# Performance work log

Hardware: AMD Instinct MI355X
Metric: run time of the kernel (lower is better)

## Reference

```python
import jax, jax.numpy as jnp
import numpy as np
from jax import lax

B, C_IN, C_OUT, K, W, H = 2, 64, 64, 9, 192, 192
EXTEND_SCOPE = 1.0
EPS = 1e-5
GN_GROUPS = C_OUT // 4


def setup_inputs() -> dict:
    key = jax.random.key(0)
    ks = jax.random.split(key, 6)
    f = jax.random.normal(ks[0], (B, C_IN, W, H), jnp.float32)
    offset_w = jax.random.normal(ks[1], (2 * K, C_IN, 3, 3), jnp.float32) * 0.02
    offset_b = jax.random.normal(ks[2], (2 * K,), jnp.float32) * 0.02
    bn_gamma = jnp.ones((2 * K,), jnp.float32)
    bn_beta = jnp.zeros((2 * K,), jnp.float32)
    conv_w = jax.random.normal(ks[3], (C_OUT, C_IN, K, 1), jnp.float32) * 0.05
    conv_b = jax.random.normal(ks[4], (C_OUT,), jnp.float32) * 0.05
    gn_gamma = jnp.ones((C_OUT,), jnp.float32)
    gn_beta = jnp.zeros((C_OUT,), jnp.float32)
    return dict(f=f, offset_w=offset_w, offset_b=offset_b, bn_gamma=bn_gamma,
                bn_beta=bn_beta, conv_w=conv_w, conv_b=conv_b,
                gn_gamma=gn_gamma, gn_beta=gn_beta)


def _forward(f, offset_w, offset_b, bn_gamma, bn_beta, conv_w, conv_b, gn_gamma, gn_beta):
    # --- offset branch: 3x3 conv -> eval-mode BatchNorm -> tanh ---
    off = lax.conv_general_dilated(f, offset_w, (1, 1), [(1, 1), (1, 1)],
                                   dimension_numbers=('NCHW', 'OIHW', 'NCHW'))
    off = off + offset_b[None, :, None, None]
    # BN eval: running_mean=0, running_var=1
    off = off / jnp.sqrt(1.0 + EPS) * bn_gamma[None, :, None, None] + bn_beta[None, :, None, None]
    off = jnp.tanh(off)
    y_off = off[:, :K]  # [B,K,W,H]; x_off (off[:, K:]) is unused when morph == 0

    # --- cumulative snake offsets along the kernel axis (morph=0 uses y only) ---
    center = K // 2
    # faithful to source: tensor starts as a detached clone; entries never
    # reassigned by the loop (index 0 and K-1 for odd K) keep raw detached offsets
    new = [lax.stop_gradient(y_off[:, i]) for i in range(K)]
    new[center] = jnp.zeros_like(new[center])
    for j in range(1, center):
        new[center + j] = new[center + j - 1] + y_off[:, center + j]
        new[center - j] = new[center - j + 1] + y_off[:, center - j]
    y_off_cum = jnp.stack(new, axis=1)  # [B,K,W,H]

    # --- deformed sampling coordinates ---
    w_idx = jnp.arange(W, dtype=jnp.float32)[None, None, :, None]
    h_idx = jnp.arange(H, dtype=jnp.float32)[None, None, None, :]
    k_off = (jnp.arange(K, dtype=jnp.float32) - center)[None, :, None, None]
    y_new = w_idx + EXTEND_SCOPE * y_off_cum              # [B,K,W,H]
    x_new = jnp.broadcast_to(h_idx + k_off, (B, K, W, H))  # [B,K,W,H]
    # torch layout: [B,K,W,H] -> [B,W,K,H] -> [B, K*W, H]
    yf = y_new.transpose(0, 2, 1, 3).reshape(-1)
    xf = x_new.transpose(0, 2, 1, 3).reshape(-1)

    # --- bilinear interpolation gather ---
    y0 = jnp.floor(yf)
    x0 = jnp.floor(xf)
    y0i = jnp.clip(y0.astype(jnp.int32), 0, W - 1)
    y1i = jnp.clip(y0.astype(jnp.int32) + 1, 0, W - 1)
    x0i = jnp.clip(x0.astype(jnp.int32), 0, H - 1)
    x1i = jnp.clip(x0.astype(jnp.int32) + 1, 0, H - 1)

    # faithful to source: base batch offset cancels, so every batch gathers
    # from batch 0's feature map
    feat0 = f[0].transpose(1, 2, 0).reshape(W * H, C_IN)  # [(w,h), C]
    va0 = feat0[y0i * H + x0i]
    vc0 = feat0[y0i * H + x1i]
    va1 = feat0[y1i * H + x0i]
    vc1 = feat0[y1i * H + x1i]

    # interpolation weights use the looser clamp [0, W] / [0, H] (source behavior)
    y0w = jnp.clip(y0, 0.0, float(W))
    y1w = jnp.clip(y0 + 1.0, 0.0, float(W))
    x0w = jnp.clip(x0, 0.0, float(H))
    x1w = jnp.clip(x0 + 1.0, 0.0, float(H))
    wa0 = (y1w - yf) * (x1w - xf)
    wc0 = (y1w - yf) * (xf - x0w)
    wa1 = (yf - y0w) * (x1w - xf)
    wc1 = (yf - y0w) * (xf - x0w)
    vals = va0 * wa0[:, None] + vc0 * wc0[:, None] + va1 * wa1[:, None] + vc1 * wc1[:, None]
    deformed = vals.reshape(B, K * W, H, C_IN).transpose(0, 3, 1, 2)  # [B,C,K*W,H]

    # --- dsc_conv_x: (K,1) kernel, (K,1) stride -> [B,C_out,W,H] ---
    z = lax.conv_general_dilated(deformed, conv_w, (K, 1), 'VALID',
                                 dimension_numbers=('NCHW', 'OIHW', 'NCHW'))
    z = z + conv_b[None, :, None, None]

    # --- GroupNorm(out_ch//4, out_ch) + ReLU ---
    zg = z.reshape(B, GN_GROUPS, -1)
    mu = zg.mean(axis=-1, keepdims=True)
    var = zg.var(axis=-1, keepdims=True)
    zg = (zg - mu) / jnp.sqrt(var + EPS)
    z = zg.reshape(B, C_OUT, W, H) * gn_gamma[None, :, None, None] + gn_beta[None, :, None, None]
    return jax.nn.relu(z)


def reference(f, offset_w, offset_b, bn_gamma, bn_beta, conv_w, conv_b, gn_gamma, gn_beta):
    return _forward(f, offset_w, offset_b, bn_gamma, bn_beta, conv_w, conv_b, gn_gamma, gn_beta)
```

## Files before the change

kernel.cpp:

```cpp
#include <hip/hip_runtime.h>

#define BB 2
#define CIN 64
#define COUT 64
#define KK 9
#define WW 192
#define HH 192
#define WH (WW*HH)
#define CENTER 4
#define NT 32
#define DEFP 584
#define GROUPS 16
constexpr float EPSV = 1e-5f;
constexpr int NPERG = 4 * WH;

typedef __attribute__((ext_vector_type(8))) short short8v;
typedef __attribute__((ext_vector_type(4))) float float4v;

__device__ __forceinline__ float bf2f(unsigned short u) {
    union { unsigned int i; float f; } x; x.i = ((unsigned int)u) << 16; return x.f;
}
__device__ __forceinline__ unsigned short f2bf(float f) {
    union { float f; unsigned int i; } x; x.f = f;
    unsigned int i = x.i;
    unsigned int r = i + 0x7FFFu + ((i >> 16) & 1u);
    return (unsigned short)(r >> 16);
}

__global__ void k_prep(const float* __restrict__ cw, const float* __restrict__ ow,
                       unsigned short* __restrict__ wtA, float* __restrict__ wl_g)
{
    int i = blockIdx.x * 256 + threadIdx.x;
    if (i < COUT * CIN * KK) {
        int o = i / 576, ck = i % 576;
        int k = ck >> 6, c = ck & 63;
        wtA[i] = f2bf(cw[o * 576 + c * 9 + k]);
    }
    int j2 = i - COUT * CIN * KK;
    if (j2 >= 0 && j2 < CIN * 9 * 12) {
        int c = j2 / 108, rem = j2 % 108, tap = rem / 12, jj = rem % 12;
        wl_g[j2] = (jj < 9) ? ow[jj * 576 + c * 9 + tap] : 0.f;
    }
}

__global__ __launch_bounds__(256) void k_tr(const float* __restrict__ f,
                                            unsigned short* __restrict__ f_t)
{
    __shared__ unsigned short tile[64][72];
    int tid = threadIdx.x;
    int y = blockIdx.y;
    int x0 = blockIdx.x * 64;
    int xl = tid & 63, cq = tid >> 6;
#pragma unroll
    for (int ci = 0; ci < 16; ++ci) {
        int c = cq * 16 + ci;
        tile[xl][c] = f2bf(f[c * WH + y * HH + x0 + xl]);
    }
    __syncthreads();
    int cp = tid & 31, xr0 = tid >> 5;
#pragma unroll
    for (int xi = 0; xi < 8; ++xi) {
        int xr = xr0 * 8 + xi;
        unsigned int val = (unsigned int)tile[xr][2 * cp] |
                           ((unsigned int)tile[xr][2 * cp + 1] << 16);
        ((unsigned int*)f_t)[(y * HH + x0 + xr) * 32 + cp] = val;
    }
}

__global__ __launch_bounds__(512) void k_offset(
    const float* __restrict__ f, const float* __restrict__ wl_g,
    const float* __restrict__ ob, const float* __restrict__ bg,
    const float* __restrict__ bb, float* __restrict__ ycum)
{
    __shared__ float4 wl4[1728];
    __shared__ float sacc[64 * 73];
    float* wl = (float*)wl4;

    int tid = threadIdx.x;
    for (int i = tid; i < 1728; i += 512)
        wl4[i] = ((const float4*)wl_g)[i];

    int hl = tid & 63, ch = tid >> 6;
    int h = blockIdx.x * 64 + hl;
    int w = blockIdx.y, b = blockIdx.z;
    __syncthreads();

    float acc[9];
#pragma unroll
    for (int j = 0; j < 9; ++j) acc[j] = 0.f;

    const float* fb = f + ((size_t)b * CIN + ch * 8) * WH;
    for (int ci = 0; ci < 8; ++ci) {
        const float* fc = fb + ci * WH;
        const float* wp = wl + (ch * 8 + ci) * 108;
#pragma unroll
        for (int dw = 0; dw < 3; ++dw) {
            int r = w + dw - 1;
            if ((unsigned)r >= WW) continue;
            const float* fr_ = fc + r * HH;
#pragma unroll
            for (int dh = 0; dh < 3; ++dh) {
                int cl = h + dh - 1;
                if ((unsigned)cl >= HH) continue;
                float v = fr_[cl];
                const float* ww = wp + (dw * 3 + dh) * 12;
                float4 wa = *(const float4*)ww;
                float4 wb2 = *(const float4*)(ww + 4);
                float w8 = ww[8];
                acc[0] += v * wa.x;  acc[1] += v * wa.y;
                acc[2] += v * wa.z;  acc[3] += v * wa.w;
                acc[4] += v * wb2.x; acc[5] += v * wb2.y;
                acc[6] += v * wb2.z; acc[7] += v * wb2.w;
                acc[8] += v * w8;
            }
        }
    }
#pragma unroll
    for (int j = 0; j < 9; ++j)
        sacc[hl * 73 + ch * 9 + j] = acc[j];
    __syncthreads();

    if (tid < 64) {
        float s[9];
#pragma unroll
        for (int j = 0; j < 9; ++j) {
            float t0 = 0.f;
#pragma unroll
            for (int c = 0; c < 8; ++c) t0 += sacc[tid * 73 + c * 9 + j];
            s[j] = t0;
        }
        const float inv = 1.0f / sqrtf(1.0f + EPSV);
        float t[9];
#pragma unroll
        for (int j = 0; j < 9; ++j)
            t[j] = tanhf((s[j] + ob[j]) * inv * bg[j] + bb[j]);
        float cum[9];
        cum[4] = 0.f;
        cum[5] = t[5]; cum[6] = cum[5] + t[6]; cum[7] = cum[6] + t[7];
        cum[3] = t[3]; cum[2] = cum[3] + t[2]; cum[1] = cum[2] + t[1];
        cum[0] = t[0]; cum[8] = t[8];
        int hh = blockIdx.x * 64 + tid;
#pragma unroll
        for (int j = 0; j < 9; ++j)
            ycum[((b * KK + j) * WW + w) * HH + hh] = cum[j];
    }
}

__global__ __launch_bounds__(256) void k_main(
    const unsigned short* __restrict__ f_t, const float* __restrict__ ycum,
    const unsigned short* __restrict__ wtA, const float* __restrict__ cb,
    float* __restrict__ zout)
{
    __shared__ unsigned short def[NT * DEFP];
    __shared__ short m_y0[KK * NT], m_y1[KK * NT], m_x[KK * NT];
    __shared__ float m_w0[KK * NT], m_w1[KK * NT];

    int tid = threadIdx.x;
    int h0blk = blockIdx.x * NT;
    int w = blockIdx.y;
    int b = blockIdx.z;
    int lane = tid & 63;
    int wid = tid >> 6;
    int lr = lane & 15;
    int lg = lane >> 4;
    int o0 = wid * 16;

    short8v afr[18];
    const unsigned short* wbase = wtA + (o0 + lr) * 576 + lg * 8;
#pragma unroll
    for (int s = 0; s < 18; ++s)
        afr[s] = *(const short8v*)(wbase + s * 32);

    for (int p = tid; p < KK * NT; p += 256) {
        int k = p / NT;
        int hl = p % NT;
        int h = h0blk + hl;
        float yf = ycum[((b * KK + k) * WW + w) * HH + h] + (float)w;
        int x = h + k - CENTER;
        float y0f = floorf(yf);
        int iy0 = (int)y0f;
        int y0i = min(max(iy0, 0), WW - 1);
        int y1i = min(max(iy0 + 1, 0), WW - 1);
        float y0w = fminf(fmaxf(y0f, 0.f), (float)WW);
        float y1w = fminf(fmaxf(y0f + 1.f, 0.f), (float)WW);
        float w0 = y1w - yf;
        float w1 = yf - y0w;
        if (x < 0 || x >= HH) { w0 = 0.f; w1 = 0.f; }
        m_y0[p] = (short)y0i;
        m_y1[p] = (short)y1i;
        m_x[p]  = (short)min(max(x, 0), HH - 1);
        m_w0[p] = w0;
        m_w1[p] = w1;
    }
    __syncthreads();

    for (int it = tid; it < KK * NT * 4; it += 256) {
        int q = it & 3;
        int p = it >> 2;
        int y0i = m_y0[p], y1i = m_y1[p], x = m_x[p];
        float w0 = m_w0[p], w1 = m_w1[p];
        const unsigned short* r0 = f_t + ((y0i * HH + x) << 6) + q * 16;
        const unsigned short* r1 = f_t + ((y1i * HH + x) << 6) + q * 16;
        short8v a0 = *(const short8v*)r0;
        short8v a1 = *(const short8v*)(r0 + 8);
        short8v c0 = *(const short8v*)r1;
        short8v c1 = *(const short8v*)(r1 + 8);
        short8v o0v, o1v;
#pragma unroll
        for (int c = 0; c < 8; ++c) {
            float v0 = bf2f((unsigned short)a0[c]) * w0 + bf2f((unsigned short)c0[c]) * w1;
            float v1 = bf2f((unsigned short)a1[c]) * w0 + bf2f((unsigned short)c1[c]) * w1;
            o0v[c] = (short)f2bf(v0);
            o1v[c] = (short)f2bf(v1);
        }
        int hl = p & 31;
        int k = p >> 5;
        unsigned short* d = &def[hl * DEFP + k * 64 + q * 16];
        *(short8v*)d = o0v;
        *(short8v*)(d + 8) = o1v;
    }
    __syncthreads();

    float4v acc0 = {0.f, 0.f, 0.f, 0.f};
    float4v acc1 = {0.f, 0.f, 0.f, 0.f};
    const unsigned short* drow0 = &def[lr * DEFP + lg * 8];
    const unsigned short* drow1 = &def[(16 + lr) * DEFP + lg * 8];
#pragma unroll
    for (int s = 0; s < 18; ++s) {
        short8v b0 = *(const short8v*)(drow0 + s * 32);
        short8v b1 = *(const short8v*)(drow1 + s * 32);
        acc0 = __builtin_amdgcn_mfma_f32_16x16x32_bf16(afr[s], b0, acc0, 0, 0, 0);
        acc1 = __builtin_amdgcn_mfma_f32_16x16x32_bf16(afr[s], b1, acc1, 0, 0, 0);
    }

    float4 cbv = *(const float4*)(cb + o0 + lg * 4);
    size_t base = ((size_t)(b * COUT + o0 + lg * 4) * WW + w) * HH + h0blk + lr;
#pragma unroll
    for (int r = 0; r < 4; ++r) {
        float bias = (r == 0) ? cbv.x : (r == 1) ? cbv.y : (r == 2) ? cbv.z : cbv.w;
        zout[base + (size_t)r * WH]      = acc0[r] + bias;
        zout[base + (size_t)r * WH + 16] = acc1[r] + bias;
    }
}

__global__ __launch_bounds__(1024) void k_gstats(const float* __restrict__ z,
                                                 float* __restrict__ ms)
{
    __shared__ float sL[16], qL[16];
    int b = blockIdx.x >> 4, g = blockIdx.x & 15;
    const float4* p = (const float4*)(z + ((size_t)b * COUT + g * 4) * WH);
    float s = 0.f, q = 0.f;
    for (int i = threadIdx.x; i < WH; i += 1024) {
        float4 v = p[i];
        s += v.x + v.y + v.z + v.w;
        q += v.x * v.x + v.y * v.y + v.z * v.z + v.w * v.w;
    }
#pragma unroll
    for (int m = 1; m < 64; m <<= 1) {
        s += __shfl_xor(s, m);
        q += __shfl_xor(q, m);
    }
    int wv = threadIdx.x >> 6;
    if ((threadIdx.x & 63) == 0) { sL[wv] = s; qL[wv] = q; }
    __syncthreads();
    if (threadIdx.x == 0) {
        float ts = 0.f, tq = 0.f;
#pragma unroll
        for (int i = 0; i < 16; ++i) { ts += sL[i]; tq += qL[i]; }
        float mean = ts / (float)NPERG;
        float var = tq / (float)NPERG - mean * mean;
        ms[b * GROUPS + g] = mean;
        ms[BB * GROUPS + b * GROUPS + g] = 1.0f / sqrtf(var + EPSV);
    }
}

__global__ __launch_bounds__(256) void k_norm(
    float* __restrict__ z, const float* __restrict__ ms,
    const float* __restrict__ gg, const float* __restrict__ gb)
{
    int i = blockIdx.x * 256 + threadIdx.x;
    const int total4 = BB * COUT * WH / 4;
    if (i >= total4) return;
    float4 v = ((float4*)z)[i];
    int idx = i * 4;
    int o = (idx / WH) % COUT;
    int b = idx / (COUT * WH);
    int g = o >> 2;
    float mean = ms[b * GROUPS + g];
    float istd = ms[BB * GROUPS + b * GROUPS + g];
    float ga = gg[o], be = gb[o];
    v.x = fmaxf((v.x - mean) * istd * ga + be, 0.f);
    v.y = fmaxf((v.y - mean) * istd * ga + be, 0.f);
    v.z = fmaxf((v.z - mean) * istd * ga + be, 0.f);
    v.w = fmaxf((v.w - mean) * istd * ga + be, 0.f);
    ((float4*)z)[i] = v;
}

extern "C" void kernel_launch(void* const* d_in, const int* in_sizes, int n_in,
                              void* d_out, int out_size, void* d_ws, size_t ws_size,
                              hipStream_t stream)
{
    const float* f  = (const float*)d_in[0];
    const float* ow = (const float*)d_in[1];
    const float* ob = (const float*)d_in[2];
    const float* bg = (const float*)d_in[3];
    const float* bb = (const float*)d_in[4];
    const float* cw = (const float*)d_in[5];
    const float* cb = (const float*)d_in[6];
    const float* gg = (const float*)d_in[7];
    const float* gb = (const float*)d_in[8];
    float* out = (float*)d_out;

    char* ws = (char*)d_ws;
    unsigned short* f_t  = (unsigned short*)ws;
    float* ycum          = (float*)(ws + 4718592);
    unsigned short* wtA  = (unsigned short*)(ws + 4718592 + 2654208);
    float* wl_g          = (float*)(ws + 4718592 + 2654208 + 73728);
    float* ms            = (float*)(ws + 4718592 + 2654208 + 73728 + 27648);

    k_prep<<<(36864 + 6912 + 255) / 256, 256, 0, stream>>>(cw, ow, wtA, wl_g);
    k_tr<<<dim3(3, WW), 256, 0, stream>>>(f, f_t);
    k_offset<<<dim3(3, WW, BB), 512, 0, stream>>>(f, wl_g, ob, bg, bb, ycum);
    k_main<<<dim3(HH / NT, WW, BB), 256, 0, stream>>>(f_t, ycum, wtA, cb, out);
    k_gstats<<<BB * GROUPS, 1024, 0, stream>>>(out, ms);
    k_norm<<<(BB * COUT * WH / 4 + 255) / 256, 256, 0, stream>>>(out, ms, gg, gb);
}
```

Measured before the change: 198.7 us.

## Fuse offset conv into deformable sampling kernel, dropping ycum buffer

Merges the offset-branch 3x3 conv with BN, tanh and cumulative sum into the main sampling+MFMA kernel. Each 32-column tile now computes its own offsets and feeds the sampling coordinates straight into shared memory, so the ycum global round trip and one kernel launch go away. The offset partial sums reuse the def shared buffer as scratch. The cost is more work per block and higher shared memory and register pressure, which may lower occupancy. Offset conv parallelism also changes from 64 to 32 columns per block with 8 channel groups.

```diff
diff --git a/kernel.cpp b/kernel.cpp
--- a/kernel.cpp
+++ b/kernel.cpp
@@ -67,66 +67,78 @@
     }
 }
 
-__global__ __launch_bounds__(512) void k_offset(
-    const float* __restrict__ f, const float* __restrict__ wl_g,
+__global__ __launch_bounds__(256) void k_fused(
+    const float* __restrict__ f, const unsigned short* __restrict__ f_t,
+    const float* __restrict__ wl_g, const unsigned short* __restrict__ wtA,
     const float* __restrict__ ob, const float* __restrict__ bg,
-    const float* __restrict__ bb, float* __restrict__ ycum)
+    const float* __restrict__ bb, const float* __restrict__ cb,
+    float* __restrict__ zout)
 {
     __shared__ float4 wl4[1728];
-    __shared__ float sacc[64 * 73];
+    __shared__ unsigned short def[NT * DEFP];
+    __shared__ short m_y0[KK * NT], m_y1[KK * NT], m_x[KK * NT];
+    __shared__ float m_w0[KK * NT], m_w1[KK * NT];
     float* wl = (float*)wl4;
+    float* part = (float*)def;
 
     int tid = threadIdx.x;
-    for (int i = tid; i < 1728; i += 512)
+    int h0 = blockIdx.x * NT;
+    int w = blockIdx.y;
+    int b = blockIdx.z;
+    int lane = tid & 63;
+    int wid = tid >> 6;
+    int lr = lane & 15;
+    int lg = lane >> 4;
+    int o0 = wid * 16;
+
+    for (int i = tid; i < 1728; i += 256)
         wl4[i] = ((const float4*)wl_g)[i];
 
-    int hl = tid & 63, ch = tid >> 6;
-    int h = blockIdx.x * 64 + hl;
-    int w = blockIdx.y, b = blockIdx.z;
-    __syncthreads();
-
+    int p = tid & 31, c8 = tid >> 5;
     float acc[9];
 #pragma unroll
     for (int j = 0; j < 9; ++j) acc[j] = 0.f;
-
-    const float* fb = f + ((size_t)b * CIN + ch * 8) * WH;
-    for (int ci = 0; ci < 8; ++ci) {
-        const float* fc = fb + ci * WH;
-        const float* wp = wl + (ch * 8 + ci) * 108;
-#pragma unroll
-        for (int dw = 0; dw < 3; ++dw) {
-            int r = w + dw - 1;
-            if ((unsigned)r >= WW) continue;
-            const float* fr_ = fc + r * HH;
-#pragma unroll
-            for (int dh = 0; dh < 3; ++dh) {
-                int cl = h + dh - 1;
-                if ((unsigned)cl >= HH) continue;
-                float v = fr_[cl];
-                const float* ww = wp + (dw * 3 + dh) * 12;
-                float4 wa = *(const float4*)ww;
-                float4 wb2 = *(const float4*)(ww + 4);
-                float w8 = ww[8];
-                acc[0] += v * wa.x;  acc[1] += v * wa.y;
-                acc[2] += v * wa.z;  acc[3] += v * wa.w;
-                acc[4] += v * wb2.x; acc[5] += v * wb2.y;
-                acc[6] += v * wb2.z; acc[7] += v * wb2.w;
-                acc[8] += v * w8;
-            }
+    const float* fb = f + ((size_t)b * CIN + c8 * 8) * WH;
+    __syncthreads();
+
+#pragma unroll
+    for (int tap = 0; tap < 9; ++tap) {
+        int r = w + tap / 3 - 1;
+        int cl = h0 + p + tap % 3 - 1;
+        if ((unsigned)r >= WW || (unsigned)cl >= HH) continue;
+        const float* src = fb + r * HH + cl;
+#pragma unroll
+        for (int cc = 0; cc < 8; ++cc) {
+            float v = src[cc * WH];
+            const float* ww = wl + (c8 * 8 + cc) * 108 + tap * 12;
+            float4 wa = *(const float4*)ww;
+            float4 wb2 = *(const float4*)(ww + 4);
+            float w8 = ww[8];
+            acc[0] += v * wa.x;  acc[1] += v * wa.y;
+            acc[2] += v * wa.z;  acc[3] += v * wa.w;
+            acc[4] += v * wb2.x; acc[5] += v * wb2.y;
+            acc[6] += v * wb2.z; acc[7] += v * wb2.w;
+            acc[8] += v * w8;
         }
     }
 #pragma unroll
     for (int j = 0; j < 9; ++j)
-        sacc[hl * 73 + ch * 9 + j] = acc[j];
-    __syncthreads();
-
-    if (tid < 64) {
+        part[(c8 * 32 + p) * 9 + j] = acc[j];
+
+    short8v afr[18];
+    const unsigned short* wbase = wtA + (o0 + lr) * 576 + lg * 8;
+#pragma unroll
+    for (int s = 0; s < 18; ++s)
+        afr[s] = *(const short8v*)(wbase + s * 32);
+    __syncthreads();
+
+    if (tid < NT) {
         float s[9];
 #pragma unroll
         for (int j = 0; j < 9; ++j) {
             float t0 = 0.f;
 #pragma unroll
-            for (int c = 0; c < 8; ++c) t0 += sacc[tid * 73 + c * 9 + j];
+            for (int g = 0; g < 8; ++g) t0 += part[(g * 32 + tid) * 9 + j];
             s[j] = t0;
         }
         const float inv = 1.0f / sqrtf(1.0f + EPSV);
@@ -139,66 +151,35 @@
         cum[5] = t[5]; cum[6] = cum[5] + t[6]; cum[7] = cum[6] + t[7];
         cum[3] = t[3]; cum[2] = cum[3] + t[2]; cum[1] = cum[2] + t[1];
         cum[0] = t[0]; cum[8] = t[8];
-        int hh = blockIdx.x * 64 + tid;
-#pragma unroll
-        for (int j = 0; j < 9; ++j)
-            ycum[((b * KK + j) * WW + w) * HH + hh] = cum[j];
-    }
-}
-
-__global__ __launch_bounds__(256) void k_main(
-    const unsigned short* __restrict__ f_t, const float* __restrict__ ycum,
-    const unsigned short* __restrict__ wtA, const float* __restrict__ cb,
-    float* __restrict__ zout)
-{
-    __shared__ unsigned short def[NT * DEFP];
-    __shared__ short m_y0[KK * NT], m_y1[KK * NT], m_x[KK * NT];
-    __shared__ float m_w0[KK * NT], m_w1[KK * NT];
-
-    int tid = threadIdx.x;
-    int h0blk = blockIdx.x * NT;
-    int w = blockIdx.y;
-    int b = blockIdx.z;
-    int lane = tid & 63;
-    int wid = tid >> 6;
-    int lr = lane & 15;
-    int lg = lane >> 4;
-    int o0 = wid * 16;
-
-    short8v afr[18];
-    const unsigned short* wbase = wtA + (o0 + lr) * 576 + lg * 8;
-#pragma unroll
-    for (int s = 0; s < 18; ++s)
-        afr[s] = *(const short8v*)(wbase + s * 32);
-
-    for (int p = tid; p < KK * NT; p += 256) {
-        int k = p / NT;
-        int hl = p % NT;
-        int h = h0blk + hl;
-        float yf = ycum[((b * KK + k) * WW + w) * HH + h] + (float)w;
-        int x = h + k - CENTER;
-        float y0f = floorf(yf);
-        int iy0 = (int)y0f;
-        int y0i = min(max(iy0, 0), WW - 1);
-        int y1i = min(max(iy0 + 1, 0), WW - 1);
-        float y0w = fminf(fmaxf(y0f, 0.f), (float)WW);
-        float y1w = fminf(fmaxf(y0f + 1.f, 0.f), (float)WW);
-        float w0 = y1w - yf;
-        float w1 = yf - y0w;
-        if (x < 0 || x >= HH) { w0 = 0.f; w1 = 0.f; }
-        m_y0[p] = (short)y0i;
-        m_y1[p] = (short)y1i;
-        m_x[p]  = (short)min(max(x, 0), HH - 1);
-        m_w0[p] = w0;
-        m_w1[p] = w1;
+        int h = h0 + tid;
+#pragma unroll
+        for (int k = 0; k < 9; ++k) {
+            float yf = cum[k] + (float)w;
+            int x = h + k - CENTER;
+            float y0f = floorf(yf);
+            int iy0 = (int)y0f;
+            int y0i = min(max(iy0, 0), WW - 1);
+            int y1i = min(max(iy0 + 1, 0), WW - 1);
+            float y0w = fminf(fmaxf(y0f, 0.f), (float)WW);
+            float y1w = fminf(fmaxf(y0f + 1.f, 0.f), (float)WW);
+            float w0 = y1w - yf;
+            float w1 = yf - y0w;
+            if (x < 0 || x >= HH) { w0 = 0.f; w1 = 0.f; }
+            int pp = k * NT + tid;
+            m_y0[pp] = (short)y0i;
+            m_y1[pp] = (short)y1i;
+            m_x[pp]  = (short)min(max(x, 0), HH - 1);
+            m_w0[pp] = w0;
+            m_w1[pp] = w1;
+        }
     }
     __syncthreads();
 
     for (int it = tid; it < KK * NT * 4; it += 256) {
         int q = it & 3;
-        int p = it >> 2;
-        int y0i = m_y0[p], y1i = m_y1[p], x = m_x[p];
-        float w0 = m_w0[p], w1 = m_w1[p];
+        int pp = it >> 2;
+        int y0i = m_y0[pp], y1i = m_y1[pp], x = m_x[pp];
+        float w0 = m_w0[pp], w1 = m_w1[pp];
         const unsigned short* r0 = f_t + ((y0i * HH + x) << 6) + q * 16;
         const unsigned short* r1 = f_t + ((y1i * HH + x) << 6) + q * 16;
         short8v a0 = *(const short8v*)r0;
@@ -213,8 +194,8 @@
             o0v[c] = (short)f2bf(v0);
             o1v[c] = (short)f2bf(v1);
         }
-        int hl = p & 31;
-        int k = p >> 5;
+        int hl = pp & 31;
+        int k = pp >> 5;
         unsigned short* d = &def[hl * DEFP + k * 64 + q * 16];
         *(short8v*)d = o0v;
         *(short8v*)(d + 8) = o1v;
@@ -234,7 +215,7 @@
     }
 
     float4 cbv = *(const float4*)(cb + o0 + lg * 4);
-    size_t base = ((size_t)(b * COUT + o0 + lg * 4) * WW + w) * HH + h0blk + lr;
+    size_t base = ((size_t)(b * COUT + o0 + lg * 4) * WW + w) * HH + h0 + lr;
 #pragma unroll
     for (int r = 0; r < 4; ++r) {
         float bias = (r == 0) ? cbv.x : (r == 1) ? cbv.y : (r == 2) ? cbv.z : cbv.w;
@@ -312,16 +293,14 @@
     float* out = (float*)d_out;
 
     char* ws = (char*)d_ws;
-    unsigned short* f_t  = (unsigned short*)ws;
-    float* ycum          = (float*)(ws + 4718592);
-    unsigned short* wtA  = (unsigned short*)(ws + 4718592 + 2654208);
-    float* wl_g          = (float*)(ws + 4718592 + 2654208 + 73728);
-    float* ms            = (float*)(ws + 4718592 + 2654208 + 73728 + 27648);
+    unsigned short* f_t = (unsigned short*)ws;
+    unsigned short* wtA = (unsigned short*)(ws + 4718592);
+    float* wl_g         = (float*)(ws + 4718592 + 73728);
+    float* ms           = (float*)(ws + 4718592 + 73728 + 27648);
 
     k_prep<<<(36864 + 6912 + 255) / 256, 256, 0, stream>>>(cw, ow, wtA, wl_g);
     k_tr<<<dim3(3, WW), 256, 0, stream>>>(f, f_t);
-    k_offset<<<dim3(3, WW, BB), 512, 0, stream>>>(f, wl_g, ob, bg, bb, ycum);
-    k_main<<<dim3(HH / NT, WW, BB), 256, 0, stream>>>(f_t, ycum, wtA, cb, out);
+    k_fused<<<dim3(HH / NT, WW, BB), 256, 0, stream>>>(f, f_t, wl_g, wtA, ob, bg, bb, cb, out);
     k_gstats<<<BB * GROUPS, 1024, 0, stream>>>(out, ms);
     k_norm<<<(BB * COUT * WH / 4 + 255) / 256, 256, 0, stream>>>(out, ms, gg, gb);
 }
```

Result: faster. 187.9 us (-5.5%).
